# Performance work log

Hardware: AMD Instinct MI355X
Metric: run time of the kernel (lower is better)

## Reference

```python
import jax, jax.numpy as jnp
import numpy as np

B, T, C, H = 2, 2048, 1024, 16
HD = C // H  # head dim = 64


def setup_inputs() -> dict:
    key = jax.random.key(0)
    ks = jax.random.split(key, 5)
    s = 1.0 / np.sqrt(C)
    return {
        "x": jax.random.normal(ks[0], (B, T, C), dtype=jnp.float32),
        "W_attn": jax.random.normal(ks[1], (3 * C, C), dtype=jnp.float32) * s,
        "b_attn": jax.random.normal(ks[2], (3 * C,), dtype=jnp.float32) * 0.02,
        "W_proj": jax.random.normal(ks[3], (C, C), dtype=jnp.float32) * s,
        "b_proj": jax.random.normal(ks[4], (C,), dtype=jnp.float32) * 0.02,
    }


def reference(x, W_attn, b_attn, W_proj, b_proj):
    Bx, Tx, Cx = x.shape
    # fused QKV projection (torch Linear: x @ W.T + b)
    qkv = x @ W_attn.T + b_attn                      # [B,T,3C]
    q, k, v = jnp.split(qkv, 3, axis=-1)
    # [B,T,C] -> [B,H,T,hd]
    q = q.reshape(Bx, Tx, H, HD).transpose(0, 2, 1, 3)
    k = k.reshape(Bx, Tx, H, HD).transpose(0, 2, 1, 3)
    v = v.reshape(Bx, Tx, H, HD).transpose(0, 2, 1, 3)
    scale = 1.0 / np.sqrt(HD)
    att = jnp.einsum('bhqd,bhkd->bhqk', q, k) * scale  # [B,H,T,T]
    causal = jnp.tril(jnp.ones((Tx, Tx), dtype=bool))
    att = jnp.where(causal[None, None], att, -jnp.inf)
    att = jax.nn.softmax(att, axis=-1)
    y = jnp.einsum('bhqk,bhkd->bhqd', att, v)          # [B,H,T,hd]
    y = y.transpose(0, 2, 1, 3).reshape(Bx, Tx, Cx)
    return y @ W_proj.T + b_proj
```

## Files before the change

### kernel.cpp

```cpp
#include <hip/hip_runtime.h>

typedef unsigned short ushort_t;
typedef __bf16 bf16x8 __attribute__((ext_vector_type(8)));
typedef float f32x4 __attribute__((ext_vector_type(4)));

__device__ inline ushort_t f2bf(float f) {
  unsigned int u = __builtin_bit_cast(unsigned int, f);
  u += 0x7fff + ((u >> 16) & 1);
  return (ushort_t)(u >> 16);
}

__device__ inline unsigned pk_bf(float a, float b) {
  unsigned ua = __builtin_bit_cast(unsigned, a);
  unsigned ub = __builtin_bit_cast(unsigned, b);
  ua += 0x7fff + ((ua >> 16) & 1);
  ub += 0x7fff + ((ub >> 16) & 1);
  return __builtin_amdgcn_perm(ub, ua, 0x07060302);
}

__device__ inline void async_ld16(const ushort_t* g, const ushort_t* l) {
  __builtin_amdgcn_global_load_lds(
      (const __attribute__((address_space(1))) void*)g,
      (__attribute__((address_space(3))) void*)l, 16, 0, 0);
}

__global__ void cvt4(const float* __restrict__ in, ushort_t* __restrict__ out, int n4) {
  int i = blockIdx.x * blockDim.x + threadIdx.x;
  if (i >= n4) return;
  float4 f = ((const float4*)in)[i];
  unsigned long long p = (unsigned long long)f2bf(f.x)
      | ((unsigned long long)f2bf(f.y) << 16)
      | ((unsigned long long)f2bf(f.z) << 32)
      | ((unsigned long long)f2bf(f.w) << 48);
  ((unsigned long long*)out)[i] = p;
}

template <int BM, int BN, int IM, int JN, int MODE>
__global__ __launch_bounds__(256) void gemm_bt(
    const ushort_t* __restrict__ A, const ushort_t* __restrict__ B,
    const float* __restrict__ bias, float* __restrict__ Cf,
    ushort_t* __restrict__ Cb, ushort_t* __restrict__ vtb,
    int M, int N, int K, int ldc, float qscale) {
  constexpr int NWN = BN / (JN * 16);
  __shared__ __align__(16) ushort_t As[BM * 64];
  __shared__ __align__(16) ushort_t Bs[BN * 64];
  const int tid = threadIdx.x;
  const int wave = tid >> 6, lane = tid & 63;
  const int quad = lane >> 4, l16 = lane & 15;
  const int r7 = l16 & 7;
  const int wr = wave / NWN, wc = wave % NWN;
  const int wm = wr * IM * 16, wn = wc * JN * 16;
  const int m0 = blockIdx.y * BM, n0 = blockIdx.x * BN;
  const ushort_t* Ag = A + (size_t)m0 * K;
  const ushort_t* Bg = B + (size_t)n0 * K;
  f32x4 acc[IM][JN] = {};

  for (int k0 = 0; k0 < K; k0 += 64) {
#pragma unroll
    for (int p = 0; p < BM / 32; ++p) {
      int ci = p * 256 + tid;
      int row = ci >> 3, ch = (ci & 7) ^ (row & 7);
      async_ld16(Ag + (size_t)row * K + k0 + ch * 8, As + (p * 256 + wave * 64) * 8);
    }
#pragma unroll
    for (int p = 0; p < BN / 32; ++p) {
      int ci = p * 256 + tid;
      int row = ci >> 3, ch = (ci & 7) ^ (row & 7);
      async_ld16(Bg + (size_t)row * K + k0 + ch * 8, Bs + (p * 256 + wave * 64) * 8);
    }
    __syncthreads();
#pragma unroll
    for (int ks = 0; ks < 2; ++ks) {
      bf16x8 af[IM], bfr[JN];
#pragma unroll
      for (int i = 0; i < IM; ++i)
        af[i] = *(const bf16x8*)(As + (wm + i * 16 + l16) * 64 + (((ks * 4 + quad) ^ r7) * 8));
#pragma unroll
      for (int j = 0; j < JN; ++j)
        bfr[j] = *(const bf16x8*)(Bs + (wn + j * 16 + l16) * 64 + (((ks * 4 + quad) ^ r7) * 8));
#pragma unroll
      for (int i = 0; i < IM; ++i)
#pragma unroll
        for (int j = 0; j < JN; ++j)
          acc[i][j] = __builtin_amdgcn_mfma_f32_16x16x32_bf16(af[i], bfr[j], acc[i][j], 0, 0, 0);
    }
    __syncthreads();
  }

  if (MODE == 1 && n0 >= 2048) {
#pragma unroll
    for (int j = 0; j < JN; ++j) {
      int col = n0 + wn + j * 16 + l16;
      int cv = col - 2048;
      float bv = bias[col];
      size_t rowbase = ((size_t)(cv >> 6)) * 64 + (cv & 63);
#pragma unroll
      for (int i = 0; i < IM; ++i) {
        int rowb = m0 + wm + i * 16 + quad * 4;
        int bb = rowb >> 11, t = rowb & 2047;
        uint2 pp;
        pp.x = pk_bf(acc[i][j][0] + bv, acc[i][j][1] + bv);
        pp.y = pk_bf(acc[i][j][2] + bv, acc[i][j][3] + bv);
        *(uint2*)(vtb + (((size_t)bb * 1024 + rowbase) * 2048 + t)) = pp;
      }
    }
    return;
  }
#pragma unroll
  for (int j = 0; j < JN; ++j) {
    int col = n0 + wn + j * 16 + l16;
    float bv = bias[col];
    float sc = (MODE == 1 && col < 1024) ? qscale : 1.0f;
#pragma unroll
    for (int i = 0; i < IM; ++i)
#pragma unroll
      for (int r = 0; r < 4; ++r) {
        int row = m0 + wm + i * 16 + quad * 4 + r;
        float v = (acc[i][j][r] + bv) * sc;
        if (MODE == 1)
          Cb[(size_t)row * ldc + col] = f2bf(v);
        else
          Cf[(size_t)row * ldc + col] = v;
      }
  }
}

__global__ __launch_bounds__(256) void flash2(
    const ushort_t* __restrict__ qk, const ushort_t* __restrict__ vt,
    ushort_t* __restrict__ y) {
  __shared__ __align__(16) ushort_t Kb[2][4096];
  __shared__ __align__(16) ushort_t Vb[2][4096];
  __shared__ __align__(16) ushort_t Ps[64 * 72];
  const int tid = threadIdx.x, wave = tid >> 6, lane = tid & 63;
  const int quad = lane >> 4, l16 = lane & 15;
  const int r7 = l16 & 7;
  const int p = blockIdx.x, bh = blockIdx.y;
  const int b = bh >> 4, h = bh & 15;
  const int bT = b * 2048;
  const int qtA = 31 - p, qtB = p;

#pragma unroll
  for (int i = 0; i < 2; ++i) {
    int ci = i * 256 + tid;
    int row = ci >> 3, ch = (ci & 7) ^ (row & 7);
    ushort_t* lk = Kb[0] + (i * 256 + wave * 64) * 8;
    ushort_t* lv = Vb[0] + (i * 256 + wave * 64) * 8;
    async_ld16(qk + (size_t)(bT + qtA * 64 + row) * 2048 + h * 64 + ch * 8, lk);
    async_ld16(qk + (size_t)(bT + qtB * 64 + row) * 2048 + h * 64 + ch * 8, lv);
  }
  __syncthreads();
  bf16x8 qaA[2], qaB[2];
#pragma unroll
  for (int ks = 0; ks < 2; ++ks) {
    int off = (wave * 16 + l16) * 64 + (((ks * 4 + quad) ^ r7) * 8);
    qaA[ks] = *(const bf16x8*)(Kb[0] + off);
    qaB[ks] = *(const bf16x8*)(Vb[0] + off);
  }
  __syncthreads();

  f32x4 oA[4] = {}, oB[4] = {};
  float lA = 0.f, lB = 0.f;

  auto stage = [&](int kt, int bsel) {
    int k0 = kt * 64;
#pragma unroll
    for (int i = 0; i < 2; ++i) {
      int ci = i * 256 + tid;
      int row = ci >> 3, ch = (ci & 7) ^ (row & 7);
      ushort_t* lk = Kb[bsel] + (i * 256 + wave * 64) * 8;
      ushort_t* lv = Vb[bsel] + (i * 256 + wave * 64) * 8;
      async_ld16(qk + (size_t)(bT + k0 + row) * 2048 + 1024 + h * 64 + ch * 8, lk);
      async_ld16(vt + (size_t)(bh * 64 + row) * 2048 + k0 + ch * 8, lv);
    }
  };

  auto process = [&](const bf16x8* qa, f32x4* o, float& l, bool diag,
                     const ushort_t* Kc, const ushort_t* Vc) {
    f32x4 s[4] = {};
#pragma unroll
    for (int ks = 0; ks < 2; ++ks) {
      bf16x8 qf = qa[ks];
#pragma unroll
      for (int j = 0; j < 4; ++j) {
        bf16x8 kf = *(const bf16x8*)(Kc + (j * 16 + l16) * 64 + (((ks * 4 + quad) ^ r7) * 8));
        s[j] = __builtin_amdgcn_mfma_f32_16x16x32_bf16(kf, qf, s[j], 0, 0, 0);
      }
    }
    if (diag) {
      int qloc = wave * 16 + l16;
#pragma unroll
      for (int j = 0; j < 4; ++j)
#pragma unroll
        for (int r = 0; r < 4; ++r)
          if (j * 16 + quad * 4 + r > qloc) s[j][r] = -1e30f;
    }
    float rs = 0.f;
#pragma unroll
    for (int j = 0; j < 4; ++j)
#pragma unroll
      for (int r = 0; r < 4; ++r) {
        float pv = exp2f(s[j][r]);
        s[j][r] = pv;
        rs += pv;
      }
    rs += __shfl_xor(rs, 16, 64);
    rs += __shfl_xor(rs, 32, 64);
    l += rs;
#pragma unroll
    for (int j = 0; j < 4; ++j) {
      uint2 pp;
      pp.x = pk_bf(s[j][0], s[j][1]);
      pp.y = pk_bf(s[j][2], s[j][3]);
      *(uint2*)(Ps + (wave * 16 + l16) * 72 + j * 16 + quad * 4) = pp;
    }
    __builtin_amdgcn_s_waitcnt(0xc07f);
#pragma unroll
    for (int ks = 0; ks < 2; ++ks) {
      bf16x8 pf = *(const bf16x8*)(Ps + (wave * 16 + l16) * 72 + ks * 32 + quad * 8);
#pragma unroll
      for (int j = 0; j < 4; ++j) {
        bf16x8 vf = *(const bf16x8*)(Vc + (j * 16 + l16) * 64 + (((ks * 4 + quad) ^ r7) * 8));
        o[j] = __builtin_amdgcn_mfma_f32_16x16x32_bf16(vf, pf, o[j], 0, 0, 0);
      }
    }
  };

  stage(0, 0);
  const int KT = qtA + 1;
  for (int kt = 0; kt < KT; ++kt) {
    const int cur = kt & 1;
    __syncthreads();
    if (kt + 1 < KT) stage(kt + 1, cur ^ 1);
    const ushort_t* Kc = Kb[cur];
    const ushort_t* Vc = Vb[cur];
    process(qaA, oA, lA, kt == qtA, Kc, Vc);
    if (kt <= qtB) process(qaB, oB, lB, kt == qtB, Kc, Vc);
  }

  auto wrt = [&](int qt, f32x4* o, float l) {
    float inv = 1.f / l;
    size_t row = (size_t)(bT + qt * 64 + wave * 16 + l16);
#pragma unroll
    for (int j = 0; j < 4; ++j) {
      uint2 pp;
      pp.x = pk_bf(o[j][0] * inv, o[j][1] * inv);
      pp.y = pk_bf(o[j][2] * inv, o[j][3] * inv);
      *(uint2*)(y + row * 1024 + h * 64 + j * 16 + quad * 4) = pp;
    }
  };
  wrt(qtA, oA, lA);
  wrt(qtB, oB, lB);
}

extern "C" void kernel_launch(void* const* d_in, const int* in_sizes, int n_in,
                              void* d_out, int out_size, void* d_ws, size_t ws_size,
                              hipStream_t stream) {
  const float* x  = (const float*)d_in[0];
  const float* Wa = (const float*)d_in[1];
  const float* ba = (const float*)d_in[2];
  const float* Wp = (const float*)d_in[3];
  const float* bp = (const float*)d_in[4];
  float* out = (float*)d_out;
  char* ws = (char*)d_ws;
  ushort_t* xb  = (ushort_t*)(ws);
  ushort_t* Wab = (ushort_t*)(ws + 8388608);
  ushort_t* Wpb = (ushort_t*)(ws + 14680064);
  ushort_t* qkb = (ushort_t*)(ws + 16777216);
  ushort_t* yb  = (ushort_t*)(ws + 33554432);
  ushort_t* vtb = (ushort_t*)(ws + 41943040);

  cvt4<<<4096 * 1024 / 4 / 256, 256, 0, stream>>>(x, xb, 4096 * 1024 / 4);
  cvt4<<<3072 * 1024 / 4 / 256, 256, 0, stream>>>(Wa, Wab, 3072 * 1024 / 4);
  cvt4<<<1024 * 1024 / 4 / 256, 256, 0, stream>>>(Wp, Wpb, 1024 * 1024 / 4);
  gemm_bt<128, 128, 4, 4, 1><<<dim3(24, 32), 256, 0, stream>>>(
      xb, Wab, ba, nullptr, qkb, vtb, 4096, 3072, 1024, 2048, 0.18033688011112042f);
  flash2<<<dim3(16, 32), 256, 0, stream>>>(qkb, vtb, yb);
  gemm_bt<64, 128, 4, 2, 0><<<dim3(8, 64), 256, 0, stream>>>(
      yb, Wpb, bp, out, nullptr, nullptr, 4096, 1024, 1024, 1024, 1.0f);
}
```

Measured before the change: 200.6 us.

## Triple-buffer GEMM and attention loads, fuse conversions, retile output projection

The GEMM now uses K-steps of 32 with three LDS buffers, issuing loads two stages ahead and waiting with partial vmcnt barriers instead of full syncthreads. The flash kernel gets triple-buffered K/V tiles plus separate Q buffers, so the first KV stages load alongside Q. The three fp32-to-bf16 conversion launches merge into one kernel, and the output projection switches to 64x64 tiles for more blocks. The aim is to hide global load latency and cut launch and barrier overhead, at the cost of more LDS per block (lower occupancy) and fragile hand-coded waitcnt immediates.

```diff
diff --git a/kernel.cpp b/kernel.cpp
--- a/kernel.cpp
+++ b/kernel.cpp
@@ -24,15 +24,30 @@
       (__attribute__((address_space(3))) void*)l, 16, 0, 0);
 }
 
-__global__ void cvt4(const float* __restrict__ in, ushort_t* __restrict__ out, int n4) {
-  int i = blockIdx.x * blockDim.x + threadIdx.x;
-  if (i >= n4) return;
-  float4 f = ((const float4*)in)[i];
+template <int IMM>
+__device__ inline void waitcnt_barrier() {
+  asm volatile("" ::: "memory");
+  __builtin_amdgcn_s_waitcnt(IMM);
+  __builtin_amdgcn_s_barrier();
+  asm volatile("" ::: "memory");
+}
+
+__global__ void cvt_all(const float* __restrict__ x, const float* __restrict__ wa,
+                        const float* __restrict__ wp, ushort_t* __restrict__ xb,
+                        ushort_t* __restrict__ wab, ushort_t* __restrict__ wpb) {
+  int i = blockIdx.x * 256 + threadIdx.x;
+  const float* src;
+  ushort_t* dst;
+  int off;
+  if (i < 1048576) { src = x; dst = xb; off = i; }
+  else if (i < 1835008) { src = wa; dst = wab; off = i - 1048576; }
+  else { src = wp; dst = wpb; off = i - 1835008; }
+  float4 f = ((const float4*)src)[off];
   unsigned long long p = (unsigned long long)f2bf(f.x)
       | ((unsigned long long)f2bf(f.y) << 16)
       | ((unsigned long long)f2bf(f.z) << 32)
       | ((unsigned long long)f2bf(f.w) << 48);
-  ((unsigned long long*)out)[i] = p;
+  ((unsigned long long*)dst)[off] = p;
 }
 
 template <int BM, int BN, int IM, int JN, int MODE>
@@ -42,49 +57,57 @@
     ushort_t* __restrict__ Cb, ushort_t* __restrict__ vtb,
     int M, int N, int K, int ldc, float qscale) {
   constexpr int NWN = BN / (JN * 16);
-  __shared__ __align__(16) ushort_t As[BM * 64];
-  __shared__ __align__(16) ushort_t Bs[BN * 64];
+  constexpr int NL = (BM + BN) / 64;
+  constexpr int WIMM = 0x0F70 | NL;
+  __shared__ __align__(16) ushort_t As[3][BM * 32];
+  __shared__ __align__(16) ushort_t Bs[3][BN * 32];
   const int tid = threadIdx.x;
   const int wave = tid >> 6, lane = tid & 63;
   const int quad = lane >> 4, l16 = lane & 15;
-  const int r7 = l16 & 7;
   const int wr = wave / NWN, wc = wave % NWN;
   const int wm = wr * IM * 16, wn = wc * JN * 16;
   const int m0 = blockIdx.y * BM, n0 = blockIdx.x * BN;
   const ushort_t* Ag = A + (size_t)m0 * K;
   const ushort_t* Bg = B + (size_t)n0 * K;
+  const int slot = (quad ^ ((l16 >> 1) & 3)) * 8;
   f32x4 acc[IM][JN] = {};
 
-  for (int k0 = 0; k0 < K; k0 += 64) {
-#pragma unroll
-    for (int p = 0; p < BM / 32; ++p) {
+  auto stage = [&](int kt, int bsel) {
+    int k0 = kt * 32;
+#pragma unroll
+    for (int p = 0; p < BM / 64; ++p) {
       int ci = p * 256 + tid;
-      int row = ci >> 3, ch = (ci & 7) ^ (row & 7);
-      async_ld16(Ag + (size_t)row * K + k0 + ch * 8, As + (p * 256 + wave * 64) * 8);
-    }
-#pragma unroll
-    for (int p = 0; p < BN / 32; ++p) {
+      int row = ci >> 2, ch = (ci & 3) ^ ((ci >> 3) & 3);
+      async_ld16(Ag + (size_t)row * K + k0 + ch * 8, As[bsel] + (p * 256 + wave * 64) * 8);
+    }
+#pragma unroll
+    for (int p = 0; p < BN / 64; ++p) {
       int ci = p * 256 + tid;
-      int row = ci >> 3, ch = (ci & 7) ^ (row & 7);
-      async_ld16(Bg + (size_t)row * K + k0 + ch * 8, Bs + (p * 256 + wave * 64) * 8);
-    }
-    __syncthreads();
-#pragma unroll
-    for (int ks = 0; ks < 2; ++ks) {
-      bf16x8 af[IM], bfr[JN];
-#pragma unroll
-      for (int i = 0; i < IM; ++i)
-        af[i] = *(const bf16x8*)(As + (wm + i * 16 + l16) * 64 + (((ks * 4 + quad) ^ r7) * 8));
+      int row = ci >> 2, ch = (ci & 3) ^ ((ci >> 3) & 3);
+      async_ld16(Bg + (size_t)row * K + k0 + ch * 8, Bs[bsel] + (p * 256 + wave * 64) * 8);
+    }
+  };
+
+  const int KT = K / 32;
+  stage(0, 0);
+  stage(1, 1);
+  for (int kt = 0; kt < KT; ++kt) {
+    waitcnt_barrier<WIMM>();
+    if (kt + 2 < KT) stage(kt + 2, (kt + 2) % 3);
+    const ushort_t* Ac = As[kt % 3];
+    const ushort_t* Bc = Bs[kt % 3];
+    bf16x8 af[IM], bfr[JN];
+#pragma unroll
+    for (int i = 0; i < IM; ++i)
+      af[i] = *(const bf16x8*)(Ac + (wm + i * 16 + l16) * 32 + slot);
+#pragma unroll
+    for (int j = 0; j < JN; ++j)
+      bfr[j] = *(const bf16x8*)(Bc + (wn + j * 16 + l16) * 32 + slot);
+#pragma unroll
+    for (int i = 0; i < IM; ++i)
 #pragma unroll
       for (int j = 0; j < JN; ++j)
-        bfr[j] = *(const bf16x8*)(Bs + (wn + j * 16 + l16) * 64 + (((ks * 4 + quad) ^ r7) * 8));
-#pragma unroll
-      for (int i = 0; i < IM; ++i)
-#pragma unroll
-        for (int j = 0; j < JN; ++j)
-          acc[i][j] = __builtin_amdgcn_mfma_f32_16x16x32_bf16(af[i], bfr[j], acc[i][j], 0, 0, 0);
-    }
-    __syncthreads();
+        acc[i][j] = __builtin_amdgcn_mfma_f32_16x16x32_bf16(af[i], bfr[j], acc[i][j], 0, 0, 0);
   }
 
   if (MODE == 1 && n0 >= 2048) {
@@ -128,8 +151,9 @@
 __global__ __launch_bounds__(256) void flash2(
     const ushort_t* __restrict__ qk, const ushort_t* __restrict__ vt,
     ushort_t* __restrict__ y) {
-  __shared__ __align__(16) ushort_t Kb[2][4096];
-  __shared__ __align__(16) ushort_t Vb[2][4096];
+  __shared__ __align__(16) ushort_t Kb[3][4096];
+  __shared__ __align__(16) ushort_t Vb[3][4096];
+  __shared__ __align__(16) ushort_t Qa[4096], Qb[4096];
   __shared__ __align__(16) ushort_t Ps[64 * 72];
   const int tid = threadIdx.x, wave = tid >> 6, lane = tid & 63;
   const int quad = lane >> 4, l16 = lane & 15;
@@ -139,40 +163,41 @@
   const int bT = b * 2048;
   const int qtA = 31 - p, qtB = p;
 
+  auto stage = [&](int kt, int bsel) {
+    int k0 = kt * 64;
+#pragma unroll
+    for (int i = 0; i < 2; ++i) {
+      int ci = i * 256 + tid;
+      int row = ci >> 3, ch = (ci & 7) ^ (row & 7);
+      async_ld16(qk + (size_t)(bT + k0 + row) * 2048 + 1024 + h * 64 + ch * 8,
+                 Kb[bsel] + (i * 256 + wave * 64) * 8);
+      async_ld16(vt + (size_t)(bh * 64 + row) * 2048 + k0 + ch * 8,
+                 Vb[bsel] + (i * 256 + wave * 64) * 8);
+    }
+  };
+
 #pragma unroll
   for (int i = 0; i < 2; ++i) {
     int ci = i * 256 + tid;
     int row = ci >> 3, ch = (ci & 7) ^ (row & 7);
-    ushort_t* lk = Kb[0] + (i * 256 + wave * 64) * 8;
-    ushort_t* lv = Vb[0] + (i * 256 + wave * 64) * 8;
-    async_ld16(qk + (size_t)(bT + qtA * 64 + row) * 2048 + h * 64 + ch * 8, lk);
-    async_ld16(qk + (size_t)(bT + qtB * 64 + row) * 2048 + h * 64 + ch * 8, lv);
-  }
-  __syncthreads();
+    async_ld16(qk + (size_t)(bT + qtA * 64 + row) * 2048 + h * 64 + ch * 8,
+               Qa + (i * 256 + wave * 64) * 8);
+    async_ld16(qk + (size_t)(bT + qtB * 64 + row) * 2048 + h * 64 + ch * 8,
+               Qb + (i * 256 + wave * 64) * 8);
+  }
+  stage(0, 0);
+  stage(1, 1);
+  waitcnt_barrier<0x0F78>();
   bf16x8 qaA[2], qaB[2];
 #pragma unroll
   for (int ks = 0; ks < 2; ++ks) {
     int off = (wave * 16 + l16) * 64 + (((ks * 4 + quad) ^ r7) * 8);
-    qaA[ks] = *(const bf16x8*)(Kb[0] + off);
-    qaB[ks] = *(const bf16x8*)(Vb[0] + off);
-  }
-  __syncthreads();
+    qaA[ks] = *(const bf16x8*)(Qa + off);
+    qaB[ks] = *(const bf16x8*)(Qb + off);
+  }
 
   f32x4 oA[4] = {}, oB[4] = {};
   float lA = 0.f, lB = 0.f;
-
-  auto stage = [&](int kt, int bsel) {
-    int k0 = kt * 64;
-#pragma unroll
-    for (int i = 0; i < 2; ++i) {
-      int ci = i * 256 + tid;
-      int row = ci >> 3, ch = (ci & 7) ^ (row & 7);
-      ushort_t* lk = Kb[bsel] + (i * 256 + wave * 64) * 8;
-      ushort_t* lv = Vb[bsel] + (i * 256 + wave * 64) * 8;
-      async_ld16(qk + (size_t)(bT + k0 + row) * 2048 + 1024 + h * 64 + ch * 8, lk);
-      async_ld16(vt + (size_t)(bh * 64 + row) * 2048 + k0 + ch * 8, lv);
-    }
-  };
 
   auto process = [&](const bf16x8* qa, f32x4* o, float& l, bool diag,
                      const ushort_t* Kc, const ushort_t* Vc) {
@@ -225,14 +250,12 @@
     }
   };
 
-  stage(0, 0);
   const int KT = qtA + 1;
   for (int kt = 0; kt < KT; ++kt) {
-    const int cur = kt & 1;
-    __syncthreads();
-    if (kt + 1 < KT) stage(kt + 1, cur ^ 1);
-    const ushort_t* Kc = Kb[cur];
-    const ushort_t* Vc = Vb[cur];
+    waitcnt_barrier<0x0F74>();
+    if (kt + 2 < KT) stage(kt + 2, (kt + 2) % 3);
+    const ushort_t* Kc = Kb[kt % 3];
+    const ushort_t* Vc = Vb[kt % 3];
     process(qaA, oA, lA, kt == qtA, Kc, Vc);
     if (kt <= qtB) process(qaB, oB, lB, kt == qtB, Kc, Vc);
   }
@@ -269,12 +292,10 @@
   ushort_t* yb  = (ushort_t*)(ws + 33554432);
   ushort_t* vtb = (ushort_t*)(ws + 41943040);
 
-  cvt4<<<4096 * 1024 / 4 / 256, 256, 0, stream>>>(x, xb, 4096 * 1024 / 4);
-  cvt4<<<3072 * 1024 / 4 / 256, 256, 0, stream>>>(Wa, Wab, 3072 * 1024 / 4);
-  cvt4<<<1024 * 1024 / 4 / 256, 256, 0, stream>>>(Wp, Wpb, 1024 * 1024 / 4);
+  cvt_all<<<8192, 256, 0, stream>>>(x, Wa, Wp, xb, Wab, Wpb);
   gemm_bt<128, 128, 4, 4, 1><<<dim3(24, 32), 256, 0, stream>>>(
       xb, Wab, ba, nullptr, qkb, vtb, 4096, 3072, 1024, 2048, 0.18033688011112042f);
   flash2<<<dim3(16, 32), 256, 0, stream>>>(qkb, vtb, yb);
-  gemm_bt<64, 128, 4, 2, 0><<<dim3(8, 64), 256, 0, stream>>>(
+  gemm_bt<64, 64, 2, 2, 0><<<dim3(16, 64), 256, 0, stream>>>(
       yb, Wpb, bp, out, nullptr, nullptr, 4096, 1024, 1024, 1024, 1.0f);
 }
```

After: 202.3 us. Within noise of the previous version (+0.9%).
